# Performance work log

Hardware: AMD Instinct MI355X
Metric: run time of the kernel (lower is better)

The kernel has to match this reference:

```python
import jax, jax.numpy as jnp
import numpy as np

BN_EPS = 1e-5
B, L, D = 16, 2048, 1024
OS = 64          # attnList[0]
NC = 256         # candidates per sample
CLASS_NUM = 8921
LAB = 1024


def setup_inputs() -> dict:
    key = jax.random.key(0)
    ks = jax.random.split(key, 8)
    scale_a = 1.0 / np.sqrt(D)
    return {
        "X": jax.random.normal(ks[0], (B, L, D), jnp.float32),
        "candidate": jax.random.randint(ks[1], (B, NC), 0, CLASS_NUM, jnp.int64),
        "a_w": jax.random.normal(ks[2], (D, OS), jnp.float32) * scale_a,
        "a_b": jnp.zeros((OS,), jnp.float32),
        "h_w": jax.random.normal(ks[3], (D, LAB), jnp.float32) * scale_a,
        "h_b": jnp.zeros((LAB,), jnp.float32),
        "bn_gamma": jax.random.uniform(ks[4], (LAB,), jnp.float32, 0.5, 1.5),
        "bn_beta": jax.random.normal(ks[5], (LAB,), jnp.float32) * 0.1,
        "bn_mean": jnp.zeros((LAB,), jnp.float32),
        "bn_var": jnp.ones((LAB,), jnp.float32),
        "labDescVec": jax.random.normal(ks[6], (CLASS_NUM, LAB), jnp.float32),
    }


def reference(X, candidate, a_w, a_b, h_w, h_b, bn_gamma, bn_beta, bn_mean, bn_var, labDescVec):
    # --- attention-pooling layer (attnList has one entry) ---
    # alpha: softmax over the sequence dim (dim=1 in torch)
    alpha = jax.nn.softmax(jnp.einsum('bld,do->blo', X, a_w) + a_b, axis=1)  # [B,L,OS]
    Xp = jnp.einsum('blo,bld->bod', alpha, X)                                # [B,OS,D]
    Xp = jnp.einsum('bod,dh->boh', Xp, h_w) + h_b                            # [B,OS,LAB]
    # BatchNorm1d over feature dim (eval mode: running stats)
    Xp = (Xp - bn_mean) * (bn_gamma / jnp.sqrt(bn_var + BN_EPS)) + bn_beta
    Xp = jax.nn.relu(Xp)  # dropout is identity at inference
    # --- candidate attention ---
    batchLabelVec = labDescVec[candidate]                                    # [B,NC,LAB]
    scores = jnp.einsum('boh,bch->boc', Xp, batchLabelVec)                   # [B,OS,NC]
    alpha2 = jax.nn.softmax(scores, axis=1)                                  # softmax over OS (dim=1)
    out = jnp.einsum('boc,boh->bch', alpha2, Xp)                             # [B,NC,LAB]
    return out
```

## Files before the change

kernel.cpp:

```cpp
#include <hip/hip_runtime.h>
#include <hip/hip_bf16.h>
#include <math.h>

#define Bb   16
#define Ll   2048
#define Dd   1024
#define OSo  64
#define NCc  256
#define LABh 1024
#define BN_EPS 1e-5f

typedef short s8v  __attribute__((ext_vector_type(8)));
typedef short s4v  __attribute__((ext_vector_type(4)));
typedef float f32x4 __attribute__((ext_vector_type(4)));

__device__ __forceinline__ short f2b(float f) {
    __hip_bfloat16 h = __float2bfloat16(f);
    short s;
    __builtin_memcpy(&s, &h, 2);
    return s;
}
__device__ __forceinline__ float b2f(short s) {
    union { unsigned u; float f; } v; v.u = ((unsigned)(unsigned short)s) << 16;
    return v.f;
}
__device__ __forceinline__ void fastbar() {
    asm volatile("s_waitcnt lgkmcnt(0)\n\ts_barrier" ::: "memory");
}
__device__ __forceinline__ int swi(int row, int kElem) {
    return (row * 128 + ((kElem * 2) ^ ((row & 7) << 4))) >> 1;
}
__device__ __forceinline__ f32x4 MF(s8v a, s8v b, f32x4 c) {
    return __builtin_amdgcn_mfma_f32_16x16x32_bf16(a, b, c, 0, 0, 0);
}

__global__ __launch_bounds__(256) void k0(const float* __restrict__ h_w,
                                          const float* __restrict__ a_w,
                                          short* __restrict__ h_wT,
                                          short* __restrict__ a_wT) {
    __shared__ float t[64][68];
    const int tid = threadIdx.x, id = blockIdx.x;
    const float* src; short* dst; int srw, d0, y0;
    if (id < 256) { src = h_w; dst = h_wT; srw = LABh; d0 = (id & 15) * 64; y0 = (id >> 4) * 64; }
    else          { src = a_w; dst = a_wT; srw = OSo;  d0 = (id - 256) * 64; y0 = 0; }
    const int r = tid >> 2, cofs = (tid & 3) * 16;
    #pragma unroll
    for (int w = 0; w < 4; ++w) {
        float4 v = *(const float4*)&src[(size_t)(d0 + r) * srw + y0 + cofs + w * 4];
        t[r][cofs + w * 4 + 0] = v.x;
        t[r][cofs + w * 4 + 1] = v.y;
        t[r][cofs + w * 4 + 2] = v.z;
        t[r][cofs + w * 4 + 3] = v.w;
    }
    __syncthreads();
    s8v o0, o1;
    #pragma unroll
    for (int e = 0; e < 8; ++e) { o0[e] = f2b(t[cofs + e][r]); o1[e] = f2b(t[cofs + 8 + e][r]); }
    *(s8v*)&dst[(size_t)(y0 + r) * Dd + d0 + cofs]     = o0;
    *(s8v*)&dst[(size_t)(y0 + r) * Dd + d0 + cofs + 8] = o1;
}

struct R1 { float4 x[4]; s8v w[2]; };

__global__ __launch_bounds__(256) void k1(const float* __restrict__ X,
                                          const short* __restrict__ a_wT,
                                          const float* __restrict__ a_b,
                                          float* __restrict__ St) {
    __shared__ __align__(16) char smem[32768];
    float (*ts)[65] = (float(*)[65])smem;
    const int tid = threadIdx.x;
    const int lane = tid & 63, wave = tid >> 6;
    const int wm = wave >> 1, wn = wave & 1;
    const int b = blockIdx.y, l0 = blockIdx.x * 64;
    const float* Xb = X + ((size_t)b * Ll + l0) * Dd;
    const int r = tid >> 2, kofs = (tid & 3) * 16;
    f32x4 acc[2][2] = {};
    R1 cur, nxt;
    #pragma unroll
    for (int w = 0; w < 2; ++w) {
        cur.x[2*w]   = *(const float4*)&Xb[(size_t)r * Dd + kofs + w * 8];
        cur.x[2*w+1] = *(const float4*)&Xb[(size_t)r * Dd + kofs + w * 8 + 4];
        cur.w[w]     = *(const s8v*)&a_wT[(size_t)r * Dd + kofs + w * 8];
    }
    #pragma unroll
    for (int t = 0; t < 16; ++t) {
        short* As = (short*)(smem + (t & 1) * 8192);
        short* Bs = (short*)(smem + 16384 + (t & 1) * 8192);
        #pragma unroll
        for (int w = 0; w < 2; ++w) {
            const float* f0 = (const float*)&cur.x[2*w];
            s8v s;
            s[0]=f2b(f0[0]); s[1]=f2b(f0[1]); s[2]=f2b(f0[2]); s[3]=f2b(f0[3]);
            s[4]=f2b(f0[4]); s[5]=f2b(f0[5]); s[6]=f2b(f0[6]); s[7]=f2b(f0[7]);
            *(s8v*)&As[swi(r, kofs + w * 8)] = s;
            *(s8v*)&Bs[swi(r, kofs + w * 8)] = cur.w[w];
        }
        fastbar();
        if (t < 15) {
            const int k0 = (t + 1) * 64;
            #pragma unroll
            for (int w = 0; w < 2; ++w) {
                nxt.x[2*w]   = *(const float4*)&Xb[(size_t)r * Dd + k0 + kofs + w * 8];
                nxt.x[2*w+1] = *(const float4*)&Xb[(size_t)r * Dd + k0 + kofs + w * 8 + 4];
                nxt.w[w]     = *(const s8v*)&a_wT[(size_t)r * Dd + k0 + kofs + w * 8];
            }
        }
        #pragma unroll
        for (int kk = 0; kk < 2; ++kk) {
            const int kb = kk * 32 + (lane >> 4) * 8;
            s8v a[2], bb[2];
            #pragma unroll
            for (int i = 0; i < 2; ++i)
                a[i] = *(const s8v*)&As[swi(wm * 32 + i * 16 + (lane & 15), kb)];
            #pragma unroll
            for (int j = 0; j < 2; ++j)
                bb[j] = *(const s8v*)&Bs[swi(wn * 32 + j * 16 + (lane & 15), kb)];
            #pragma unroll
            for (int i = 0; i < 2; ++i)
                #pragma unroll
                for (int j = 0; j < 2; ++j)
                    acc[i][j] = MF(a[i], bb[j], acc[i][j]);
        }
        if (t < 15) cur = nxt;
    }
    __syncthreads();
    #pragma unroll
    for (int i = 0; i < 2; ++i)
        #pragma unroll
        for (int j = 0; j < 2; ++j)
            #pragma unroll
            for (int rr = 0; rr < 4; ++rr)
                ts[wm * 32 + i * 16 + (lane >> 4) * 4 + rr][wn * 32 + j * 16 + (lane & 15)] = acc[i][j][rr];
    __syncthreads();
    const int o = tid >> 2, lofs = (tid & 3) * 16;
    const float bias = a_b[o];
    float* Sp = St + ((size_t)b * OSo + o) * Ll + l0 + lofs;
    #pragma unroll
    for (int w = 0; w < 4; ++w) {
        float4 v;
        v.x = ts[lofs + w * 4 + 0][o] + bias;
        v.y = ts[lofs + w * 4 + 1][o] + bias;
        v.z = ts[lofs + w * 4 + 2][o] + bias;
        v.w = ts[lofs + w * 4 + 3][o] + bias;
        *(float4*)&Sp[w * 4] = v;
    }
}

__global__ __launch_bounds__(256) void k2(const float* __restrict__ St, short* __restrict__ aBf) {
    __shared__ float row[Ll];
    __shared__ float red[8];
    const float* p = St + (size_t)blockIdx.x * Ll;
    short* ab = aBf + (size_t)blockIdx.x * Ll;
    const int tid = threadIdx.x;
    const int wave = tid >> 6, lane = tid & 63;
    float m = -1e30f;
    for (int i = tid; i < Ll; i += 256) { float v = p[i]; row[i] = v; m = fmaxf(m, v); }
    #pragma unroll
    for (int off = 32; off; off >>= 1) m = fmaxf(m, __shfl_down(m, off));
    if (lane == 0) red[wave] = m;
    __syncthreads();
    if (tid == 0) red[4] = fmaxf(fmaxf(red[0], red[1]), fmaxf(red[2], red[3]));
    __syncthreads();
    const float M = red[4];
    float s = 0.f;
    for (int i = tid; i < Ll; i += 256) { float e = __expf(row[i] - M); row[i] = e; s += e; }
    __syncthreads();
    #pragma unroll
    for (int off = 32; off; off >>= 1) s += __shfl_down(s, off);
    if (lane == 0) red[wave] = s;
    __syncthreads();
    if (tid == 0) red[4] = 1.f / (red[0] + red[1] + red[2] + red[3]);
    __syncthreads();
    const float inv = red[4];
    for (int i = tid; i < Ll; i += 256) ab[i] = f2b(row[i] * inv);
}

struct R3 { s8v al[2]; float4 xv[4]; };

__global__ __launch_bounds__(256) void k3(const float* __restrict__ X,
                                          const short* __restrict__ aBf,
                                          float* __restrict__ XpP) {
    __shared__ __align__(16) char smem[32768];
    float (*ts)[68] = (float(*)[68])smem;
    const int tid = threadIdx.x;
    const int lane = tid & 63, wave = tid >> 6;
    const int wm = wave >> 1, wn = wave & 1;
    const int id = blockIdx.x;
    const int slot = id >> 3;
    const int b = (id & 7) * 2 + (slot >> 5);
    const int inner = slot & 31;
    const int dt = inner & 15, z = inner >> 4;
    const int d0 = dt * 64;
    const float* Xb = X + (size_t)b * Ll * Dd;
    const short* ab = aBf + (size_t)b * OSo * Ll;
    float* outP = XpP + (size_t)z * ((size_t)Bb * OSo * Dd);
    f32x4 acc[2][2] = {};
    const int arow = tid >> 2, akofs = (tid & 3) * 16;
    const int lq = tid & 15, dq = tid >> 4;
    const int lbase = z * 1024;
    R3 cur, nxt;
    #pragma unroll
    for (int w = 0; w < 2; ++w)
        cur.al[w] = *(const s8v*)&ab[(size_t)arow * Ll + lbase + akofs + w * 8];
    #pragma unroll
    for (int i = 0; i < 4; ++i)
        cur.xv[i] = *(const float4*)&Xb[(size_t)(lbase + lq * 4 + i) * Dd + d0 + dq * 4];
    #pragma unroll
    for (int t = 0; t < 16; ++t) {
        short* Aal = (short*)(smem + (t & 1) * 8192);
        short* Xs  = (short*)(smem + 16384 + (t & 1) * 8192);
        #pragma unroll
        for (int w = 0; w < 2; ++w)
            *(s8v*)&Aal[swi(arow, akofs + w * 8)] = cur.al[w];
        {
            const float* f = (const float*)cur.xv;
            #pragma unroll
            for (int j = 0; j < 4; ++j) {
                const int rowd = dq * 4 + j;
                s4v sj;
                sj[0] = f2b(f[0 * 4 + j]);
                sj[1] = f2b(f[1 * 4 + j]);
                sj[2] = f2b(f[2 * 4 + j]);
                sj[3] = f2b(f[3 * 4 + j]);
                *(s4v*)&Xs[swi(rowd, lq * 4)] = sj;
            }
        }
        fastbar();
        if (t < 15) {
            const int l0 = lbase + (t + 1) * 64;
            #pragma unroll
            for (int w = 0; w < 2; ++w)
                nxt.al[w] = *(const s8v*)&ab[(size_t)arow * Ll + l0 + akofs + w * 8];
            #pragma unroll
            for (int i = 0; i < 4; ++i)
                nxt.xv[i] = *(const float4*)&Xb[(size_t)(l0 + lq * 4 + i) * Dd + d0 + dq * 4];
        }
        #pragma unroll
        for (int kk = 0; kk < 2; ++kk) {
            const int kb = kk * 32 + (lane >> 4) * 8;
            s8v a[2], bb[2];
            #pragma unroll
            for (int i = 0; i < 2; ++i)
                a[i] = *(const s8v*)&Aal[swi(wm * 32 + i * 16 + (lane & 15), kb)];
            #pragma unroll
            for (int j = 0; j < 2; ++j)
                bb[j] = *(const s8v*)&Xs[swi(wn * 32 + j * 16 + (lane & 15), kb)];
            #pragma unroll
            for (int i = 0; i < 2; ++i)
                #pragma unroll
                for (int j = 0; j < 2; ++j)
                    acc[i][j] = MF(a[i], bb[j], acc[i][j]);
        }
        if (t < 15) cur = nxt;
    }
    __syncthreads();
    #pragma unroll
    for (int i = 0; i < 2; ++i)
        #pragma unroll
        for (int j = 0; j < 2; ++j)
            #pragma unroll
            for (int rr = 0; rr < 4; ++rr)
                ts[wm * 32 + i * 16 + (lane >> 4) * 4 + rr][wn * 32 + j * 16 + (lane & 15)] = acc[i][j][rr];
    __syncthreads();
    const int o = tid >> 2, dofs = (tid & 3) * 16;
    float* op = outP + ((size_t)b * OSo + o) * Dd + d0 + dofs;
    #pragma unroll
    for (int w = 0; w < 4; ++w)
        *(float4*)&op[w * 4] = *(float4*)&ts[o][dofs + w * 4];
}

struct R4 { float4 p[8]; s8v w[2]; };

__global__ __launch_bounds__(256) void k4(const float* __restrict__ XpP,
                                          const short* __restrict__ h_wT,
                                          const float* __restrict__ h_b,
                                          const float* __restrict__ gamma,
                                          const float* __restrict__ beta,
                                          const float* __restrict__ mean,
                                          const float* __restrict__ var,
                                          short* __restrict__ Xh) {
    __shared__ __align__(16) char smem[32768];
    short* tsb = (short*)smem;
    const int tid = threadIdx.x, lane = tid & 63, wave = tid >> 6;
    const int wm = wave >> 1, wn = wave & 1;
    const int h0 = blockIdx.x * 64, m0 = blockIdx.y * 64;
    const int r = tid >> 2, kofs = (tid & 3) * 16;
    const size_t ZS = (size_t)Bb * OSo * Dd;
    f32x4 acc[2][2] = {};
    R4 cur, nxt;
    #pragma unroll
    for (int w = 0; w < 2; ++w) {
        const float* p0 = XpP + (size_t)(m0 + r) * Dd + kofs + w * 8;
        cur.p[w*4+0] = *(const float4*)&p0[0];
        cur.p[w*4+1] = *(const float4*)&p0[4];
        cur.p[w*4+2] = *(const float4*)&p0[ZS];
        cur.p[w*4+3] = *(const float4*)&p0[ZS + 4];
        cur.w[w]     = *(const s8v*)&h_wT[(size_t)(h0 + r) * Dd + kofs + w * 8];
    }
    #pragma unroll
    for (int t = 0; t < 16; ++t) {
        short* As = (short*)(smem + (t & 1) * 8192);
        short* Bs = (short*)(smem + 16384 + (t & 1) * 8192);
        #pragma unroll
        for (int w = 0; w < 2; ++w) {
            const float* f0 = (const float*)&cur.p[w*4];
            const float* f1 = (const float*)&cur.p[w*4+2];
            s8v s;
            #pragma unroll
            for (int e = 0; e < 8; ++e) s[e] = f2b(f0[e] + f1[e]);
            *(s8v*)&As[swi(r, kofs + w * 8)] = s;
            *(s8v*)&Bs[swi(r, kofs + w * 8)] = cur.w[w];
        }
        fastbar();
        if (t < 15) {
            const int k0 = (t + 1) * 64;
            #pragma unroll
            for (int w = 0; w < 2; ++w) {
                const float* p0 = XpP + (size_t)(m0 + r) * Dd + k0 + kofs + w * 8;
                nxt.p[w*4+0] = *(const float4*)&p0[0];
                nxt.p[w*4+1] = *(const float4*)&p0[4];
                nxt.p[w*4+2] = *(const float4*)&p0[ZS];
                nxt.p[w*4+3] = *(const float4*)&p0[ZS + 4];
                nxt.w[w]     = *(const s8v*)&h_wT[(size_t)(h0 + r) * Dd + k0 + kofs + w * 8];
            }
        }
        #pragma unroll
        for (int kk = 0; kk < 2; ++kk) {
            const int kb = kk * 32 + (lane >> 4) * 8;
            s8v a[2], bb[2];
            #pragma unroll
            for (int i = 0; i < 2; ++i)
                a[i] = *(const s8v*)&As[swi(wm * 32 + i * 16 + (lane & 15), kb)];
            #pragma unroll
            for (int j = 0; j < 2; ++j)
                bb[j] = *(const s8v*)&Bs[swi(wn * 32 + j * 16 + (lane & 15), kb)];
            #pragma unroll
            for (int i = 0; i < 2; ++i)
                #pragma unroll
                for (int j = 0; j < 2; ++j)
                    acc[i][j] = MF(a[i], bb[j], acc[i][j]);
        }
        if (t < 15) cur = nxt;
    }
    __syncthreads();
    #pragma unroll
    for (int j = 0; j < 2; ++j) {
        const int h = h0 + wn * 32 + j * 16 + (lane & 15);
        const float sc = gamma[h] * rsqrtf(var[h] + BN_EPS);
        const float of = (h_b[h] - mean[h]) * sc + beta[h];
        #pragma unroll
        for (int i = 0; i < 2; ++i)
            #pragma unroll
            for (int rr = 0; rr < 4; ++rr) {
                const int ml = wm * 32 + i * 16 + (lane >> 4) * 4 + rr;
                tsb[ml * 64 + wn * 32 + j * 16 + (lane & 15)] = f2b(fmaxf(0.f, acc[i][j][rr] * sc + of));
            }
    }
    __syncthreads();
    #pragma unroll
    for (int w = 0; w < 2; ++w)
        *(s8v*)&Xh[(size_t)(m0 + r) * LABh + h0 + kofs + w * 8] = *(const s8v*)&tsb[r * 64 + kofs + w * 8];
}

struct R5 { float4 ld[4]; s8v xh[2]; };

__global__ __launch_bounds__(256) void k5(const int* __restrict__ cand,
                                          const float* __restrict__ labD,
                                          const short* __restrict__ Xh,
                                          float* __restrict__ scP) {
    __shared__ __align__(16) char smem[33024];
    float (*ts)[68] = (float(*)[68])smem;
    int* cidx = (int*)(smem + 32768);
    const int tid = threadIdx.x, lane = tid & 63, wave = tid >> 6;
    const int wm = wave >> 1, wn = wave & 1;
    const int b = blockIdx.y;
    const int ct = blockIdx.x & 3, z = blockIdx.x >> 2;
    const int c0 = ct * 64;
    const int kbase = z * 256;
    if (tid < 64) cidx[tid] = cand[b * NCc + c0 + tid];
    __syncthreads();
    const int r = tid >> 2, kofs = (tid & 3) * 16;
    const int ci = cidx[r];
    const float* lrow = labD + (size_t)ci * LABh + kbase;
    const short* xrow = Xh + (size_t)(b * OSo + r) * LABh + kbase;
    f32x4 acc[2][2] = {};
    R5 cur, nxt;
    #pragma unroll
    for (int w = 0; w < 2; ++w) {
        cur.ld[2*w]   = *(const float4*)&lrow[kofs + w * 8];
        cur.ld[2*w+1] = *(const float4*)&lrow[kofs + w * 8 + 4];
        cur.xh[w]     = *(const s8v*)&xrow[kofs + w * 8];
    }
    #pragma unroll
    for (int t = 0; t < 4; ++t) {
        short* As = (short*)(smem + (t & 1) * 8192);
        short* Bs = (short*)(smem + 16384 + (t & 1) * 8192);
        #pragma unroll
        for (int w = 0; w < 2; ++w) {
            const float* f0 = (const float*)&cur.ld[2*w];
            s8v s;
            #pragma unroll
            for (int e = 0; e < 8; ++e) s[e] = f2b(f0[e]);
            *(s8v*)&As[swi(r, kofs + w * 8)] = s;
            *(s8v*)&Bs[swi(r, kofs + w * 8)] = cur.xh[w];
        }
        fastbar();
        if (t < 3) {
            const int k0 = (t + 1) * 64;
            #pragma unroll
            for (int w = 0; w < 2; ++w) {
                nxt.ld[2*w]   = *(const float4*)&lrow[k0 + kofs + w * 8];
                nxt.ld[2*w+1] = *(const float4*)&lrow[k0 + kofs + w * 8 + 4];
                nxt.xh[w]     = *(const s8v*)&xrow[k0 + kofs + w * 8];
            }
        }
        #pragma unroll
        for (int kk = 0; kk < 2; ++kk) {
            const int kb = kk * 32 + (lane >> 4) * 8;
            s8v a[2], bb[2];
            #pragma unroll
            for (int i = 0; i < 2; ++i)
                a[i] = *(const s8v*)&As[swi(wm * 32 + i * 16 + (lane & 15), kb)];
            #pragma unroll
            for (int j = 0; j < 2; ++j)
                bb[j] = *(const s8v*)&Bs[swi(wn * 32 + j * 16 + (lane & 15), kb)];
            #pragma unroll
            for (int i = 0; i < 2; ++i)
                #pragma unroll
                for (int j = 0; j < 2; ++j)
                    acc[i][j] = MF(a[i], bb[j], acc[i][j]);
        }
        if (t < 3) cur = nxt;
    }
    __syncthreads();
    #pragma unroll
    for (int i = 0; i < 2; ++i)
        #pragma unroll
        for (int j = 0; j < 2; ++j)
            #pragma unroll
            for (int rr = 0; rr < 4; ++rr)
                ts[wm * 32 + i * 16 + (lane >> 4) * 4 + rr][wn * 32 + j * 16 + (lane & 15)] = acc[i][j][rr];
    __syncthreads();
    const int oofs = (tid & 3) * 16;
    float* sp = scP + (size_t)z * ((size_t)Bb * NCc * OSo)
                    + ((size_t)b * NCc + c0 + r) * OSo + oofs;
    #pragma unroll
    for (int w = 0; w < 4; ++w)
        *(float4*)&sp[w * 4] = *(float4*)&ts[r][oofs + w * 4];
}

__global__ __launch_bounds__(256) void k6(const float* __restrict__ scP,
                                          const short* __restrict__ Xh,
                                          float* __restrict__ out) {
    __shared__ float al[8][64];
    const int tid = threadIdx.x;
    const int id = blockIdx.x;
    const int slot = id >> 3;
    const int b = (id & 7) * 2 + (slot >> 5);
    const int c0 = (slot & 31) * 8;
    const size_t ZS = (size_t)Bb * NCc * OSo;
    {
        const int cl = tid >> 5, t32 = tid & 31;
        const float* srow = scP + ((size_t)b * NCc + c0 + cl) * OSo;
        float v[2];
        float m = -1e30f;
        #pragma unroll
        for (int j = 0; j < 2; ++j) {
            const int o = t32 + j * 32;
            v[j] = srow[o] + srow[ZS + o] + srow[2 * ZS + o] + srow[3 * ZS + o];
            m = fmaxf(m, v[j]);
        }
        #pragma unroll
        for (int off = 16; off; off >>= 1) m = fmaxf(m, __shfl_xor(m, off, 32));
        float s = 0.f;
        #pragma unroll
        for (int j = 0; j < 2; ++j) { v[j] = __expf(v[j] - m); s += v[j]; }
        #pragma unroll
        for (int off = 16; off; off >>= 1) s += __shfl_xor(s, off, 32);
        float inv = 1.f / s;
        #pragma unroll
        for (int j = 0; j < 2; ++j) al[cl][t32 + j * 32] = v[j] * inv;
    }
    __syncthreads();
    const short* xb = Xh + (size_t)b * OSo * LABh;
    float acc[8][4] = {};
    for (int o = 0; o < OSo; ++o) {
        s4v xv = *(const s4v*)&xb[(size_t)o * LABh + tid * 4];
        const float x0 = b2f(xv[0]), x1 = b2f(xv[1]), x2 = b2f(xv[2]), x3 = b2f(xv[3]);
        #pragma unroll
        for (int c = 0; c < 8; ++c) {
            const float w = al[c][o];
            acc[c][0] += w * x0; acc[c][1] += w * x1; acc[c][2] += w * x2; acc[c][3] += w * x3;
        }
    }
    #pragma unroll
    for (int c = 0; c < 8; ++c) {
        float4 v; v.x = acc[c][0]; v.y = acc[c][1]; v.z = acc[c][2]; v.w = acc[c][3];
        *(float4*)&out[((size_t)b * NCc + c0 + c) * LABh + tid * 4] = v;
    }
}

extern "C" void kernel_launch(void* const* d_in, const int* in_sizes, int n_in,
                              void* d_out, int out_size, void* d_ws, size_t ws_size,
                              hipStream_t stream) {
    (void)in_sizes; (void)n_in; (void)out_size; (void)ws_size;
    const float* X      = (const float*)d_in[0];
    const int*   cand   = (const int*)  d_in[1];
    const float* a_w    = (const float*)d_in[2];
    const float* a_b    = (const float*)d_in[3];
    const float* h_w    = (const float*)d_in[4];
    const float* h_b    = (const float*)d_in[5];
    const float* gamma  = (const float*)d_in[6];
    const float* beta   = (const float*)d_in[7];
    const float* mean   = (const float*)d_in[8];
    const float* var    = (const float*)d_in[9];
    const float* labDesc= (const float*)d_in[10];
    float* outp = (float*)d_out;

    char* ws = (char*)d_ws;
    float* St   = (float*)ws;
    float* XpP  = St;
    short* aBf  = (short*)(ws + ((size_t)8  << 20));
    short* Xh   = (short*)(ws + ((size_t)12 << 20));
    float* scP  = (float*)(ws + ((size_t)14 << 20));
    short* a_wT = (short*)(ws + ((size_t)18 << 20));
    short* h_wT = (short*)(ws + ((size_t)19 << 20));

    k0 <<<272,          256, 0, stream>>>(h_w, a_w, h_wT, a_wT);
    k1 <<<dim3(32, 16), 256, 0, stream>>>(X, a_wT, a_b, St);
    k2 <<<Bb * OSo,     256, 0, stream>>>(St, aBf);
    k3 <<<512,          256, 0, stream>>>(X, aBf, XpP);
    k4 <<<dim3(16, 16), 256, 0, stream>>>(XpP, h_wT, h_b, gamma, beta, mean, var, Xh);
    k5 <<<dim3(16, 16), 256, 0, stream>>>(cand, labDesc, Xh, scP);
    k6 <<<512,          256, 0, stream>>>(scP, Xh, outp);
}
```

Before: 110.9 us.

## Load MFMA operands directly from global memory, dropping LDS staging in GEMM kernels

Kernels k1, k4 and k5 now load their MFMA A and B fragments straight from global memory into registers, converting fp32 to bf16 in place. This removes the double-buffered shared-memory tiles, the swizzled LDS writes and reads, and the per-tile barriers. In exchange, every wave re-reads overlapping rows from global memory and L2, so operand reuse across waves in a block is lost. Each lane also issues narrower, strided loads instead of coalesced tile loads, and the software prefetch is replaced by loop unrolling.

```diff
diff --git a/kernel.cpp b/kernel.cpp
--- a/kernel.cpp
+++ b/kernel.cpp
@@ -60,70 +60,41 @@
     *(s8v*)&dst[(size_t)(y0 + r) * Dd + d0 + cofs + 8] = o1;
 }
 
-struct R1 { float4 x[4]; s8v w[2]; };
-
 __global__ __launch_bounds__(256) void k1(const float* __restrict__ X,
                                           const short* __restrict__ a_wT,
                                           const float* __restrict__ a_b,
                                           float* __restrict__ St) {
-    __shared__ __align__(16) char smem[32768];
-    float (*ts)[65] = (float(*)[65])smem;
-    const int tid = threadIdx.x;
-    const int lane = tid & 63, wave = tid >> 6;
+    __shared__ float ts[64][65];
+    const int tid = threadIdx.x, lane = tid & 63, wave = tid >> 6;
     const int wm = wave >> 1, wn = wave & 1;
     const int b = blockIdx.y, l0 = blockIdx.x * 64;
+    const int rA = wm * 32 + (lane & 15);
+    const int rB = wn * 32 + (lane & 15);
+    const int klane = (lane >> 4) * 8;
     const float* Xb = X + ((size_t)b * Ll + l0) * Dd;
-    const int r = tid >> 2, kofs = (tid & 3) * 16;
     f32x4 acc[2][2] = {};
-    R1 cur, nxt;
-    #pragma unroll
-    for (int w = 0; w < 2; ++w) {
-        cur.x[2*w]   = *(const float4*)&Xb[(size_t)r * Dd + kofs + w * 8];
-        cur.x[2*w+1] = *(const float4*)&Xb[(size_t)r * Dd + kofs + w * 8 + 4];
-        cur.w[w]     = *(const s8v*)&a_wT[(size_t)r * Dd + kofs + w * 8];
-    }
-    #pragma unroll
-    for (int t = 0; t < 16; ++t) {
-        short* As = (short*)(smem + (t & 1) * 8192);
-        short* Bs = (short*)(smem + 16384 + (t & 1) * 8192);
-        #pragma unroll
-        for (int w = 0; w < 2; ++w) {
-            const float* f0 = (const float*)&cur.x[2*w];
+    #pragma unroll 4
+    for (int k0 = 0; k0 < Dd; k0 += 32) {
+        s8v a[2], bb[2];
+        #pragma unroll
+        for (int i = 0; i < 2; ++i) {
+            const float* p = &Xb[(size_t)(rA + i * 16) * Dd + k0 + klane];
+            float4 v0 = *(const float4*)p;
+            float4 v1 = *(const float4*)(p + 4);
             s8v s;
-            s[0]=f2b(f0[0]); s[1]=f2b(f0[1]); s[2]=f2b(f0[2]); s[3]=f2b(f0[3]);
-            s[4]=f2b(f0[4]); s[5]=f2b(f0[5]); s[6]=f2b(f0[6]); s[7]=f2b(f0[7]);
-            *(s8v*)&As[swi(r, kofs + w * 8)] = s;
-            *(s8v*)&Bs[swi(r, kofs + w * 8)] = cur.w[w];
-        }
-        fastbar();
-        if (t < 15) {
-            const int k0 = (t + 1) * 64;
-            #pragma unroll
-            for (int w = 0; w < 2; ++w) {
-                nxt.x[2*w]   = *(const float4*)&Xb[(size_t)r * Dd + k0 + kofs + w * 8];
-                nxt.x[2*w+1] = *(const float4*)&Xb[(size_t)r * Dd + k0 + kofs + w * 8 + 4];
-                nxt.w[w]     = *(const s8v*)&a_wT[(size_t)r * Dd + k0 + kofs + w * 8];
-            }
-        }
-        #pragma unroll
-        for (int kk = 0; kk < 2; ++kk) {
-            const int kb = kk * 32 + (lane >> 4) * 8;
-            s8v a[2], bb[2];
-            #pragma unroll
-            for (int i = 0; i < 2; ++i)
-                a[i] = *(const s8v*)&As[swi(wm * 32 + i * 16 + (lane & 15), kb)];
+            s[0]=f2b(v0.x); s[1]=f2b(v0.y); s[2]=f2b(v0.z); s[3]=f2b(v0.w);
+            s[4]=f2b(v1.x); s[5]=f2b(v1.y); s[6]=f2b(v1.z); s[7]=f2b(v1.w);
+            a[i] = s;
+        }
+        #pragma unroll
+        for (int j = 0; j < 2; ++j)
+            bb[j] = *(const s8v*)&a_wT[(size_t)(rB + j * 16) * Dd + k0 + klane];
+        #pragma unroll
+        for (int i = 0; i < 2; ++i)
             #pragma unroll
             for (int j = 0; j < 2; ++j)
-                bb[j] = *(const s8v*)&Bs[swi(wn * 32 + j * 16 + (lane & 15), kb)];
-            #pragma unroll
-            for (int i = 0; i < 2; ++i)
-                #pragma unroll
-                for (int j = 0; j < 2; ++j)
-                    acc[i][j] = MF(a[i], bb[j], acc[i][j]);
-        }
-        if (t < 15) cur = nxt;
-    }
-    __syncthreads();
+                acc[i][j] = MF(a[i], bb[j], acc[i][j]);
+    }
     #pragma unroll
     for (int i = 0; i < 2; ++i)
         #pragma unroll
@@ -269,8 +240,6 @@
         *(float4*)&op[w * 4] = *(float4*)&ts[o][dofs + w * 4];
 }
 
-struct R4 { float4 p[8]; s8v w[2]; };
-
 __global__ __launch_bounds__(256) void k4(const float* __restrict__ XpP,
                                           const short* __restrict__ h_wT,
                                           const float* __restrict__ h_b,
@@ -279,70 +248,39 @@
                                           const float* __restrict__ mean,
                                           const float* __restrict__ var,
                                           short* __restrict__ Xh) {
-    __shared__ __align__(16) char smem[32768];
-    short* tsb = (short*)smem;
+    __shared__ short tsb[64 * 64];
     const int tid = threadIdx.x, lane = tid & 63, wave = tid >> 6;
     const int wm = wave >> 1, wn = wave & 1;
     const int h0 = blockIdx.x * 64, m0 = blockIdx.y * 64;
-    const int r = tid >> 2, kofs = (tid & 3) * 16;
+    const int rA = wm * 32 + (lane & 15);
+    const int rB = wn * 32 + (lane & 15);
+    const int klane = (lane >> 4) * 8;
     const size_t ZS = (size_t)Bb * OSo * Dd;
     f32x4 acc[2][2] = {};
-    R4 cur, nxt;
-    #pragma unroll
-    for (int w = 0; w < 2; ++w) {
-        const float* p0 = XpP + (size_t)(m0 + r) * Dd + kofs + w * 8;
-        cur.p[w*4+0] = *(const float4*)&p0[0];
-        cur.p[w*4+1] = *(const float4*)&p0[4];
-        cur.p[w*4+2] = *(const float4*)&p0[ZS];
-        cur.p[w*4+3] = *(const float4*)&p0[ZS + 4];
-        cur.w[w]     = *(const s8v*)&h_wT[(size_t)(h0 + r) * Dd + kofs + w * 8];
-    }
-    #pragma unroll
-    for (int t = 0; t < 16; ++t) {
-        short* As = (short*)(smem + (t & 1) * 8192);
-        short* Bs = (short*)(smem + 16384 + (t & 1) * 8192);
-        #pragma unroll
-        for (int w = 0; w < 2; ++w) {
-            const float* f0 = (const float*)&cur.p[w*4];
-            const float* f1 = (const float*)&cur.p[w*4+2];
+    #pragma unroll 4
+    for (int k0 = 0; k0 < Dd; k0 += 32) {
+        s8v a[2], bb[2];
+        #pragma unroll
+        for (int i = 0; i < 2; ++i) {
+            const float* p0 = XpP + (size_t)(m0 + rA + i * 16) * Dd + k0 + klane;
+            float4 u0 = *(const float4*)p0;
+            float4 u1 = *(const float4*)(p0 + 4);
+            float4 w0 = *(const float4*)(p0 + ZS);
+            float4 w1 = *(const float4*)(p0 + ZS + 4);
             s8v s;
-            #pragma unroll
-            for (int e = 0; e < 8; ++e) s[e] = f2b(f0[e] + f1[e]);
-            *(s8v*)&As[swi(r, kofs + w * 8)] = s;
-            *(s8v*)&Bs[swi(r, kofs + w * 8)] = cur.w[w];
-        }
-        fastbar();
-        if (t < 15) {
-            const int k0 = (t + 1) * 64;
-            #pragma unroll
-            for (int w = 0; w < 2; ++w) {
-                const float* p0 = XpP + (size_t)(m0 + r) * Dd + k0 + kofs + w * 8;
-                nxt.p[w*4+0] = *(const float4*)&p0[0];
-                nxt.p[w*4+1] = *(const float4*)&p0[4];
-                nxt.p[w*4+2] = *(const float4*)&p0[ZS];
-                nxt.p[w*4+3] = *(const float4*)&p0[ZS + 4];
-                nxt.w[w]     = *(const s8v*)&h_wT[(size_t)(h0 + r) * Dd + k0 + kofs + w * 8];
-            }
-        }
-        #pragma unroll
-        for (int kk = 0; kk < 2; ++kk) {
-            const int kb = kk * 32 + (lane >> 4) * 8;
-            s8v a[2], bb[2];
-            #pragma unroll
-            for (int i = 0; i < 2; ++i)
-                a[i] = *(const s8v*)&As[swi(wm * 32 + i * 16 + (lane & 15), kb)];
+            s[0]=f2b(u0.x+w0.x); s[1]=f2b(u0.y+w0.y); s[2]=f2b(u0.z+w0.z); s[3]=f2b(u0.w+w0.w);
+            s[4]=f2b(u1.x+w1.x); s[5]=f2b(u1.y+w1.y); s[6]=f2b(u1.z+w1.z); s[7]=f2b(u1.w+w1.w);
+            a[i] = s;
+        }
+        #pragma unroll
+        for (int j = 0; j < 2; ++j)
+            bb[j] = *(const s8v*)&h_wT[(size_t)(h0 + rB + j * 16) * Dd + k0 + klane];
+        #pragma unroll
+        for (int i = 0; i < 2; ++i)
             #pragma unroll
             for (int j = 0; j < 2; ++j)
-                bb[j] = *(const s8v*)&Bs[swi(wn * 32 + j * 16 + (lane & 15), kb)];
-            #pragma unroll
-            for (int i = 0; i < 2; ++i)
-                #pragma unroll
-                for (int j = 0; j < 2; ++j)
-                    acc[i][j] = MF(a[i], bb[j], acc[i][j]);
-        }
-        if (t < 15) cur = nxt;
-    }
-    __syncthreads();
+                acc[i][j] = MF(a[i], bb[j], acc[i][j]);
+    }
     #pragma unroll
     for (int j = 0; j < 2; ++j) {
         const int h = h0 + wn * 32 + j * 16 + (lane & 15);
@@ -357,20 +295,18 @@
             }
     }
     __syncthreads();
+    const int r = tid >> 2, kofs = (tid & 3) * 16;
     #pragma unroll
     for (int w = 0; w < 2; ++w)
         *(s8v*)&Xh[(size_t)(m0 + r) * LABh + h0 + kofs + w * 8] = *(const s8v*)&tsb[r * 64 + kofs + w * 8];
 }
-
-struct R5 { float4 ld[4]; s8v xh[2]; };
 
 __global__ __launch_bounds__(256) void k5(const int* __restrict__ cand,
                                           const float* __restrict__ labD,
                                           const short* __restrict__ Xh,
                                           float* __restrict__ scP) {
-    __shared__ __align__(16) char smem[33024];
-    float (*ts)[68] = (float(*)[68])smem;
-    int* cidx = (int*)(smem + 32768);
+    __shared__ float ts[64][68];
+    __shared__ int cidx[64];
     const int tid = threadIdx.x, lane = tid & 63, wave = tid >> 6;
     const int wm = wave >> 1, wn = wave & 1;
     const int b = blockIdx.y;
@@ -379,60 +315,36 @@
     const int kbase = z * 256;
     if (tid < 64) cidx[tid] = cand[b * NCc + c0 + tid];
     __syncthreads();
-    const int r = tid >> 2, kofs = (tid & 3) * 16;
-    const int ci = cidx[r];
-    const float* lrow = labD + (size_t)ci * LABh + kbase;
-    const short* xrow = Xh + (size_t)(b * OSo + r) * LABh + kbase;
+    const int rA = wm * 32 + (lane & 15);
+    const int rB = wn * 32 + (lane & 15);
+    const int klane = (lane >> 4) * 8;
+    const int ciA0 = cidx[rA], ciA1 = cidx[rA + 16];
+    const float* lr0 = labD + (size_t)ciA0 * LABh + kbase + klane;
+    const float* lr1 = labD + (size_t)ciA1 * LABh + kbase + klane;
+    const short* xb  = Xh + (size_t)b * OSo * LABh + kbase + klane;
     f32x4 acc[2][2] = {};
-    R5 cur, nxt;
-    #pragma unroll
-    for (int w = 0; w < 2; ++w) {
-        cur.ld[2*w]   = *(const float4*)&lrow[kofs + w * 8];
-        cur.ld[2*w+1] = *(const float4*)&lrow[kofs + w * 8 + 4];
-        cur.xh[w]     = *(const s8v*)&xrow[kofs + w * 8];
-    }
-    #pragma unroll
-    for (int t = 0; t < 4; ++t) {
-        short* As = (short*)(smem + (t & 1) * 8192);
-        short* Bs = (short*)(smem + 16384 + (t & 1) * 8192);
-        #pragma unroll
-        for (int w = 0; w < 2; ++w) {
-            const float* f0 = (const float*)&cur.ld[2*w];
+    #pragma unroll 2
+    for (int k0 = 0; k0 < 256; k0 += 32) {
+        s8v a[2], bb[2];
+        #pragma unroll
+        for (int i = 0; i < 2; ++i) {
+            const float* p = (i == 0 ? lr0 : lr1) + k0;
+            float4 v0 = *(const float4*)p;
+            float4 v1 = *(const float4*)(p + 4);
             s8v s;
-            #pragma unroll
-            for (int e = 0; e < 8; ++e) s[e] = f2b(f0[e]);
-            *(s8v*)&As[swi(r, kofs + w * 8)] = s;
-            *(s8v*)&Bs[swi(r, kofs + w * 8)] = cur.xh[w];
-        }
-        fastbar();
-        if (t < 3) {
-            const int k0 = (t + 1) * 64;
-            #pragma unroll
-            for (int w = 0; w < 2; ++w) {
-                nxt.ld[2*w]   = *(const float4*)&lrow[k0 + kofs + w * 8];
-                nxt.ld[2*w+1] = *(const float4*)&lrow[k0 + kofs + w * 8 + 4];
-                nxt.xh[w]     = *(const s8v*)&xrow[k0 + kofs + w * 8];
-            }
-        }
-        #pragma unroll
-        for (int kk = 0; kk < 2; ++kk) {
-            const int kb = kk * 32 + (lane >> 4) * 8;
-            s8v a[2], bb[2];
-            #pragma unroll
-            for (int i = 0; i < 2; ++i)
-                a[i] = *(const s8v*)&As[swi(wm * 32 + i * 16 + (lane & 15), kb)];
+            s[0]=f2b(v0.x); s[1]=f2b(v0.y); s[2]=f2b(v0.z); s[3]=f2b(v0.w);
+            s[4]=f2b(v1.x); s[5]=f2b(v1.y); s[6]=f2b(v1.z); s[7]=f2b(v1.w);
+            a[i] = s;
+        }
+        #pragma unroll
+        for (int j = 0; j < 2; ++j)
+            bb[j] = *(const s8v*)&xb[(size_t)(rB + j * 16) * LABh + k0];
+        #pragma unroll
+        for (int i = 0; i < 2; ++i)
             #pragma unroll
             for (int j = 0; j < 2; ++j)
-                bb[j] = *(const s8v*)&Bs[swi(wn * 32 + j * 16 + (lane & 15), kb)];
-            #pragma unroll
-            for (int i = 0; i < 2; ++i)
-                #pragma unroll
-                for (int j = 0; j < 2; ++j)
-                    acc[i][j] = MF(a[i], bb[j], acc[i][j]);
-        }
-        if (t < 3) cur = nxt;
-    }
-    __syncthreads();
+                acc[i][j] = MF(a[i], bb[j], acc[i][j]);
+    }
     #pragma unroll
     for (int i = 0; i < 2; ++i)
         #pragma unroll
@@ -441,7 +353,7 @@
             for (int rr = 0; rr < 4; ++rr)
                 ts[wm * 32 + i * 16 + (lane >> 4) * 4 + rr][wn * 32 + j * 16 + (lane & 15)] = acc[i][j][rr];
     __syncthreads();
-    const int oofs = (tid & 3) * 16;
+    const int r = tid >> 2, oofs = (tid & 3) * 16;
     float* sp = scP + (size_t)z * ((size_t)Bb * NCc * OSo)
                     + ((size_t)b * NCc + c0 + r) * OSo + oofs;
     #pragma unroll
```

Measured after the change: 160.0 us. 1.44x slower.
